# Kernel optimization log

Measured on AMD Instinct MI355X. Metric: run time of the kernel, lower is better.

The kernel has to match this reference:

```python
import jax, jax.numpy as jnp
import numpy as np
from functools import partial

EPS = 1e-5
ROPE_THETA = 10000.0
TOP_K = 2


def rmsnorm(x, w):
    # x: [..., d]
    var = jnp.mean(x * x, axis=-1, keepdims=True)
    return x * jax.lax.rsqrt(var + EPS) * w


def apply_rope(x):
    # x: [B, S, H, dh]
    B, S, H, dh = x.shape
    inv_freq = 1.0 / (ROPE_THETA ** (jnp.arange(0, dh, 2, dtype=jnp.float32) / dh))
    ang = jnp.arange(S, dtype=jnp.float32)[:, None] * inv_freq[None, :]  # [S, dh/2]
    cos = jnp.cos(ang)[None, :, None, :]
    sin = jnp.sin(ang)[None, :, None, :]
    x1 = x[..., 0::2]
    x2 = x[..., 1::2]
    r1 = x1 * cos - x2 * sin
    r2 = x1 * sin + x2 * cos
    return jnp.stack([r1, r2], axis=-1).reshape(x.shape)


def setup_inputs() -> dict:
    key = jax.random.key(0)
    B, S, D, H, E = 4, 2048, 512, 8, 8
    Hf = 4 * D  # expert FFN hidden
    ks = jax.random.split(key, 10)
    s = 0.02
    return {
        "x": jax.random.normal(ks[0], (B, S, D), dtype=jnp.float32),
        "attn_norm_w": jnp.ones((D,), dtype=jnp.float32),
        "wq": jax.random.normal(ks[1], (D, D), dtype=jnp.float32) * s,
        "wk": jax.random.normal(ks[2], (D, D), dtype=jnp.float32) * s,
        "wv": jax.random.normal(ks[3], (D, D), dtype=jnp.float32) * s,
        "wo": jax.random.normal(ks[4], (D, D), dtype=jnp.float32) * s,
        "ffn_norm_w": jnp.ones((D,), dtype=jnp.float32),
        "router_w": jax.random.normal(ks[5], (D, E), dtype=jnp.float32) * s,
        "w1": jax.random.normal(ks[6], (E, D, Hf), dtype=jnp.float32) * s,
        "w2": jax.random.normal(ks[7], (E, Hf, D), dtype=jnp.float32) * s,
    }


def mha_rope(xn, wq, wk, wv, wo, num_heads):
    B, S, D = xn.shape
    dh = D // num_heads
    q = (xn @ wq).reshape(B, S, num_heads, dh)
    k = (xn @ wk).reshape(B, S, num_heads, dh)
    v = (xn @ wv).reshape(B, S, num_heads, dh)
    q = apply_rope(q)
    k = apply_rope(k)
    scores = jnp.einsum("bqhd,bkhd->bhqk", q, k) / jnp.sqrt(jnp.float32(dh))
    causal = jnp.tril(jnp.ones((S, S), dtype=bool))
    scores = jnp.where(causal[None, None], scores, jnp.float32(-1e9))
    attn = jax.nn.softmax(scores, axis=-1)
    out = jnp.einsum("bhqk,bkhd->bqhd", attn, v).reshape(B, S, D)
    return out @ wo


def moe_ffn(hn, router_w, w1, w2):
    # hn: [B, S, D] -> tokens [T, D]; top-2 routed expert MLPs (GELU)
    B, S, D = hn.shape
    E = router_w.shape[1]
    t = hn.reshape(B * S, D)
    T = t.shape[0]
    logits = t @ router_w                      # [T, E]
    probs = jax.nn.softmax(logits, axis=-1)
    vals, idx = jax.lax.top_k(probs, TOP_K)    # [T, k]
    gates = vals / jnp.sum(vals, axis=-1, keepdims=True)
    gates_dense = jnp.zeros((T, E), dtype=t.dtype).at[
        jnp.arange(T)[:, None], idx
    ].add(gates)                               # sparse gates, zero for unrouted
    out = jnp.zeros_like(t)
    for e in range(E):  # fixed small expert loop
        ge = gates_dense[:, e:e + 1]           # [T, 1]
        h = jax.nn.gelu(t @ w1[e], approximate=False)
        out = out + ge * (h @ w2[e])
    return out.reshape(B, S, D)


def reference(x, attn_norm_w, wq, wk, wv, wo, ffn_norm_w, router_w, w1, w2):
    num_heads = 8
    h = x + mha_rope(rmsnorm(x, attn_norm_w), wq, wk, wv, wo, num_heads)
    out = h + moe_ffn(rmsnorm(h, ffn_norm_w), router_w, w1, w2)
    return out
```

## Files before the change

### kernel.cpp

```cpp
#include <hip/hip_runtime.h>

#define BATCH 4
#define SEQ 2048
#define DMODEL 512
#define NHEAD 8
#define DHEAD 64
#define NEXP 8
#define DFF 2048
#define TOK (BATCH*SEQ)

typedef __attribute__((ext_vector_type(8))) short short8;
typedef __attribute__((ext_vector_type(8))) _Float16 half8;
typedef __attribute__((ext_vector_type(4))) float f32x4;
typedef unsigned short u16;

__device__ inline f32x4 zero4(){ f32x4 z = {0.f,0.f,0.f,0.f}; return z; }
__device__ inline u16 f2bf(float f){ unsigned u; __builtin_memcpy(&u,&f,4); u = (u + 0x7fffu + ((u>>16)&1u)) >> 16; return (u16)u; }
__device__ inline unsigned pack2(_Float16 a, _Float16 b){
  unsigned short ua, ub; __builtin_memcpy(&ua,&a,2); __builtin_memcpy(&ub,&b,2);
  return (unsigned)ua | ((unsigned)ub<<16);
}

__global__ __launch_bounds__(256) void k_tc_bf(const float* __restrict__ W, u16* __restrict__ Wt, int R, int C){
  __shared__ float tile[32][33];
  long e = blockIdx.z;
  const float* Wp = W + e*(long)R*C;
  u16* Op = Wt + e*(long)R*C;
  int c0 = blockIdx.x*32, r0 = blockIdx.y*32;
  int tx = threadIdx.x & 31, ty = threadIdx.x >> 5;
  #pragma unroll
  for (int i=0;i<4;i++){ int r = ty*4+i; tile[r][tx] = Wp[(long)(r0+r)*C + c0+tx]; }
  __syncthreads();
  #pragma unroll
  for (int i=0;i<4;i++){ int cc = ty*4+i; Op[(long)(c0+cc)*R + r0+tx] = f2bf(tile[tx][cc]); }
}

__global__ __launch_bounds__(256) void k_tc_split(const float* __restrict__ W, _Float16* __restrict__ H, _Float16* __restrict__ L, int R, int C){
  __shared__ float tile[32][33];
  int c0 = blockIdx.x*32, r0 = blockIdx.y*32;
  int tx = threadIdx.x & 31, ty = threadIdx.x >> 5;
  #pragma unroll
  for (int i=0;i<4;i++){ int r = ty*4+i; tile[r][tx] = W[(long)(r0+r)*C + c0+tx]; }
  __syncthreads();
  #pragma unroll
  for (int i=0;i<4;i++){
    int cc = ty*4+i;
    float v = tile[tx][cc];
    _Float16 hi = (_Float16)v;
    long o = (long)(c0+cc)*R + r0+tx;
    H[o] = hi; L[o] = (_Float16)(v - (float)hi);
  }
}

__global__ __launch_bounds__(256) void k_vtrans(const _Float16* __restrict__ vh, const _Float16* __restrict__ vl,
                                                _Float16* __restrict__ vth, _Float16* __restrict__ vtl){
  __shared__ _Float16 t[32][33];
  int bh = blockIdx.z;
  int b = bh>>3, h = bh&7;
  int s0 = blockIdx.x*32, d0 = blockIdx.y*32;
  int tx = threadIdx.x & 31, ty = threadIdx.x >> 5;
  const _Float16* src = vh; _Float16* dst = vth;
  #pragma unroll
  for (int pass=0; pass<2; pass++){
    #pragma unroll
    for (int i=0;i<4;i++){
      int sl = ty*4+i;
      t[sl][tx] = src[((long)b*SEQ + s0+sl)*DMODEL + h*64 + d0 + tx];
    }
    __syncthreads();
    #pragma unroll
    for (int i=0;i<4;i++){
      int dl = ty*4+i;
      dst[((long)bh*64 + d0+dl)*SEQ + s0 + tx] = t[tx][dl];
    }
    __syncthreads();
    src = vl; dst = vtl;
  }
}

__global__ __launch_bounds__(256) void k_rmsnorm_split(const float* __restrict__ x, const float* __restrict__ w,
                                                       _Float16* __restrict__ oh, _Float16* __restrict__ ol){
  int row = blockIdx.x*4 + (threadIdx.x>>6);
  int lane = threadIdx.x & 63;
  const float4* xr = (const float4*)(x + (long)row*DMODEL);
  float4 a = xr[lane*2], b = xr[lane*2+1];
  float ss = a.x*a.x+a.y*a.y+a.z*a.z+a.w*a.w + b.x*b.x+b.y*b.y+b.z*b.z+b.w*b.w;
  #pragma unroll
  for (int o=32;o;o>>=1) ss += __shfl_xor(ss, o);
  float sc = rsqrtf(ss*(1.0f/DMODEL) + 1e-5f);
  const float4* wr = (const float4*)w;
  float4 wa = wr[lane*2], wb = wr[lane*2+1];
  float v[8] = {a.x*sc*wa.x, a.y*sc*wa.y, a.z*sc*wa.z, a.w*sc*wa.w,
                b.x*sc*wb.x, b.y*sc*wb.y, b.z*sc*wb.z, b.w*sc*wb.w};
  half8 hv, lv;
  #pragma unroll
  for (int j=0;j<8;j++){ _Float16 hi = (_Float16)v[j]; hv[j] = hi; lv[j] = (_Float16)(v[j]-(float)hi); }
  long off = (long)row*DMODEL + lane*8;
  *(half8*)(oh + off) = hv;
  *(half8*)(ol + off) = lv;
}

__global__ __launch_bounds__(256) void k_rmsnorm_bf(const float* __restrict__ x, const float* __restrict__ w, u16* __restrict__ o){
  int row = blockIdx.x*4 + (threadIdx.x>>6);
  int lane = threadIdx.x & 63;
  const float4* xr = (const float4*)(x + (long)row*DMODEL);
  float4 a = xr[lane*2], b = xr[lane*2+1];
  float ss = a.x*a.x+a.y*a.y+a.z*a.z+a.w*a.w + b.x*b.x+b.y*b.y+b.z*b.z+b.w*b.w;
  #pragma unroll
  for (int ofs=32;ofs;ofs>>=1) ss += __shfl_xor(ss, ofs);
  float sc = rsqrtf(ss*(1.0f/DMODEL) + 1e-5f);
  const float4* wr = (const float4*)w;
  float4 wa = wr[lane*2], wb = wr[lane*2+1];
  short8 ov;
  ov[0]=(short)f2bf(a.x*sc*wa.x); ov[1]=(short)f2bf(a.y*sc*wa.y);
  ov[2]=(short)f2bf(a.z*sc*wa.z); ov[3]=(short)f2bf(a.w*sc*wa.w);
  ov[4]=(short)f2bf(b.x*sc*wb.x); ov[5]=(short)f2bf(b.y*sc*wb.y);
  ov[6]=(short)f2bf(b.z*sc*wb.z); ov[7]=(short)f2bf(b.w*sc*wb.w);
  *(short8*)(o + (long)row*DMODEL + lane*8) = ov;
}

__global__ __launch_bounds__(256) void k_rope_tab(float2* __restrict__ tab){
  int idx = blockIdx.x*256 + threadIdx.x;
  int s = idx>>5, i = idx&31;
  float invf = powf(10000.0f, -(float)(2*i)*(1.0f/64.0f));
  float ang = (float)s * invf;
  tab[idx] = make_float2(cosf(ang), sinf(ang));
}

template<int EPI>
__global__ __launch_bounds__(256) void k_gemm_split(
    const _Float16* __restrict__ Ah, const _Float16* __restrict__ Al,
    const _Float16* __restrict__ Bh, const _Float16* __restrict__ Bl,
    _Float16* __restrict__ oh, _Float16* __restrict__ ol,
    float* __restrict__ of1, float* __restrict__ of2,
    const float* __restrict__ extra, const float2* __restrict__ tab,
    int M, int N, int K)
{
  __shared__ _Float16 lA[128*64];
  __shared__ _Float16 lB[128*64];
  const int mb = blockIdx.x*128, nb = blockIdx.y*128;
  const int tid = threadIdx.x, lane = tid&63, wid = tid>>6;
  const int wr = wid>>1, wc = wid&1;
  const int fr = lane&15, fq = lane>>4;
  const int srow = tid>>3, sch = tid&7;
  f32x4 acc[4][4];
  #pragma unroll
  for (int mi=0;mi<4;mi++)
    #pragma unroll
    for (int ni=0;ni<4;ni++) acc[mi][ni] = zero4();

  for (int kt=0; kt<K; kt+=32){
    half8 sa[4], sb[4];
    #pragma unroll
    for (int i=0;i<4;i++){
      int row = i*32 + srow;
      const _Float16* pa = (sch<4) ? Ah : Al;
      const _Float16* pb = (sch<4) ? Bh : Bl;
      sa[i] = *(const half8*)(pa + (long)(mb+row)*K + kt + (sch&3)*8);
      sb[i] = *(const half8*)(pb + (long)(nb+row)*K + kt + (sch&3)*8);
    }
    __syncthreads();
    #pragma unroll
    for (int i=0;i<4;i++){
      int row = i*32 + srow;
      int byt = row*128 + ((sch ^ (row&7))<<4);
      *(half8*)((char*)lA + byt) = sa[i];
      *(half8*)((char*)lB + byt) = sb[i];
    }
    __syncthreads();
    half8 ah[4], al[4], bh[4], bl[4];
    #pragma unroll
    for (int mi=0;mi<4;mi++){
      int row = wr*64 + mi*16 + fr; int m7 = row&7; const char* rb = (const char*)lA + row*128;
      ah[mi] = *(const half8*)(rb + (((fq  ) ^ m7)<<4));
      al[mi] = *(const half8*)(rb + (((fq+4) ^ m7)<<4));
    }
    #pragma unroll
    for (int ni=0;ni<4;ni++){
      int row = wc*64 + ni*16 + fr; int m7 = row&7; const char* rb = (const char*)lB + row*128;
      bh[ni] = *(const half8*)(rb + (((fq  ) ^ m7)<<4));
      bl[ni] = *(const half8*)(rb + (((fq+4) ^ m7)<<4));
    }
    __builtin_amdgcn_s_setprio(1);
    #pragma unroll
    for (int mi=0;mi<4;mi++)
      #pragma unroll
      for (int ni=0;ni<4;ni++){
        acc[mi][ni] = __builtin_amdgcn_mfma_f32_16x16x32_f16(ah[mi], bh[ni], acc[mi][ni], 0,0,0);
        acc[mi][ni] = __builtin_amdgcn_mfma_f32_16x16x32_f16(ah[mi], bl[ni], acc[mi][ni], 0,0,0);
        acc[mi][ni] = __builtin_amdgcn_mfma_f32_16x16x32_f16(al[mi], bh[ni], acc[mi][ni], 0,0,0);
      }
    __builtin_amdgcn_s_setprio(0);
  }
  #pragma unroll
  for (int mi=0;mi<4;mi++)
    #pragma unroll
    for (int ni=0;ni<4;ni++)
      #pragma unroll
      for (int r=0;r<4;r++){
        int row = mb + wr*64 + mi*16 + fq*4 + r;
        int col = nb + wc*64 + ni*16 + fr;
        long off = (long)row*N + col;
        float v = acc[mi][ni][r];
        if (EPI==0){
          float v2 = __shfl_xor(v, 1);
          float2 cs = tab[(row & (SEQ-1))*32 + ((col&63)>>1)];
          float o = (col&1) ? (v2*cs.y + v*cs.x) : (v*cs.x - v2*cs.y);
          _Float16 hi = (_Float16)o;
          oh[off] = hi; ol[off] = (_Float16)(o - (float)hi);
        } else if (EPI==1){
          _Float16 hi = (_Float16)v;
          oh[off] = hi; ol[off] = (_Float16)(v - (float)hi);
        } else {
          float hv = extra[off] + v;
          of1[off] = hv; of2[off] = hv;
        }
      }
}

__global__ __launch_bounds__(256) void k_flash(
    const _Float16* __restrict__ Qh, const _Float16* __restrict__ Ql,
    const _Float16* __restrict__ Kh, const _Float16* __restrict__ Kl,
    const _Float16* __restrict__ Vth, const _Float16* __restrict__ Vtl,
    _Float16* __restrict__ Oh, _Float16* __restrict__ Ol)
{
  __shared__ _Float16 lK[64*128];
  __shared__ _Float16 lV[64*128];
  __shared__ _Float16 lP[4*2304];
  const int pidx = blockIdx.x, bh = blockIdx.y;
  const int b = bh>>3, hh = bh&7;
  const int tid = threadIdx.x, lane = tid&63, wid = tid>>6;
  const int fr = lane&15, fq = lane>>4;
  const long base = ((long)b*SEQ)*DMODEL + hh*DHEAD;
  const long vtb  = (long)bh*DHEAD*SEQ;
  const int srow = tid>>4, sch = tid&15;
  const unsigned pw = wid*2304;

  for (int pass=0; pass<2; pass++){
    const int qt = pass ? (SEQ/64-1-pidx) : pidx;
    const int q0 = qt*64, qw = q0 + wid*16;
    half8 qfh[2], qfl[2];
    #pragma unroll
    for (int kk=0;kk<2;kk++){
      long o = base + (long)(qw+fr)*DMODEL + kk*32 + fq*8;
      qfh[kk] = *(const half8*)(Qh + o);
      qfl[kk] = *(const half8*)(Ql + o);
    }
    f32x4 oacc[4];
    #pragma unroll
    for (int i=0;i<4;i++) oacc[i] = zero4();
    float mrow[4], lrow[4];
    #pragma unroll
    for (int r=0;r<4;r++){ mrow[r] = -__builtin_inff(); lrow[r] = 0.f; }

    for (int kvt=0; kvt<=qt; kvt++){
      int k0 = kvt*64;
      half8 kreg[4], vreg[4];
      #pragma unroll
      for (int i=0;i<4;i++){
        int row = i*16 + srow;
        const _Float16* ks = (sch<8) ? Kh : Kl;
        kreg[i] = *(const half8*)(ks + base + (long)(k0+row)*DMODEL + (sch&7)*8);
        const _Float16* vs = (sch<8) ? Vth : Vtl;
        vreg[i] = *(const half8*)(vs + vtb + (long)row*SEQ + k0 + (sch&7)*8);
      }
      __syncthreads();
      #pragma unroll
      for (int i=0;i<4;i++){
        int row = i*16 + srow;
        int slot = ((sch ^ (row&15))<<4);
        *(half8*)((char*)lK + row*256 + slot) = kreg[i];
        *(half8*)((char*)lV + row*256 + slot) = vreg[i];
      }
      __syncthreads();
      f32x4 sc[4];
      __builtin_amdgcn_s_setprio(1);
      #pragma unroll
      for (int ns=0;ns<4;ns++){
        f32x4 a = zero4();
        #pragma unroll
        for (int kk=0;kk<2;kk++){
          int row = ns*16 + fr; int m15 = row&15; const char* rb = (const char*)lK + row*256;
          half8 kfh = *(const half8*)(rb + (((kk*4+fq)   ^ m15)<<4));
          half8 kfl = *(const half8*)(rb + (((kk*4+fq+8) ^ m15)<<4));
          a = __builtin_amdgcn_mfma_f32_16x16x32_f16(qfh[kk], kfh, a, 0,0,0);
          a = __builtin_amdgcn_mfma_f32_16x16x32_f16(qfh[kk], kfl, a, 0,0,0);
          a = __builtin_amdgcn_mfma_f32_16x16x32_f16(qfl[kk], kfh, a, 0,0,0);
        }
        sc[ns] = a;
      }
      __builtin_amdgcn_s_setprio(0);
      float pmax[4];
      #pragma unroll
      for (int r=0;r<4;r++) pmax[r] = -__builtin_inff();
      #pragma unroll
      for (int ns=0;ns<4;ns++)
        #pragma unroll
        for (int r=0;r<4;r++){
          int kvp = k0 + ns*16 + fr;
          int qp  = qw + fq*4 + r;
          float s = sc[ns][r]*0.125f;
          if (kvp > qp) s = -1e30f;
          sc[ns][r] = s;
          pmax[r] = fmaxf(pmax[r], s);
        }
      #pragma unroll
      for (int o=1;o<16;o<<=1)
        #pragma unroll
        for (int r=0;r<4;r++) pmax[r] = fmaxf(pmax[r], __shfl_xor(pmax[r], o));
      float sf[4], rsum[4] = {0,0,0,0};
      #pragma unroll
      for (int r=0;r<4;r++){
        float mn = fmaxf(mrow[r], pmax[r]);
        sf[r] = expf(mrow[r]-mn);
        mrow[r] = mn;
      }
      #pragma unroll
      for (int ns=0;ns<4;ns++)
        #pragma unroll
        for (int r=0;r<4;r++){
          float pv = expf(sc[ns][r]-mrow[r]);
          rsum[r] += pv;
          float pv2 = __shfl_xor(pv, 1);
          float e0 = (fr&1)? pv2 : pv;
          float e1 = (fr&1)? pv : pv2;
          _Float16 f0 = (_Float16)e0, f1 = (_Float16)e1;
          unsigned word;
          if (fr&1) word = pack2((_Float16)(e0-(float)f0), (_Float16)(e1-(float)f1));
          else      word = pack2(f0, f1);
          unsigned eo = pw + ((fr&1)? 1152u:0u) + (unsigned)((fq*4+r)*72 + ns*16 + (fr&~1));
          *(unsigned*)((char*)lP + eo*2) = word;
        }
      #pragma unroll
      for (int o=1;o<16;o<<=1)
        #pragma unroll
        for (int r=0;r<4;r++) rsum[r] += __shfl_xor(rsum[r], o);
      #pragma unroll
      for (int r=0;r<4;r++) lrow[r] = lrow[r]*sf[r] + rsum[r];
      #pragma unroll
      for (int dt=0;dt<4;dt++)
        #pragma unroll
        for (int r=0;r<4;r++) oacc[dt][r] *= sf[r];
      __builtin_amdgcn_s_setprio(1);
      #pragma unroll
      for (int kk=0;kk<2;kk++){
        const char* pb = (const char*)lP + (pw + (unsigned)(fr*72 + kk*32))*2;
        half8 pfh = *(const half8*)(pb + fq*16);
        half8 pfl = *(const half8*)(pb + 2304 + fq*16);
        #pragma unroll
        for (int dt=0;dt<4;dt++){
          int row = dt*16 + fr; int m15 = row&15; const char* vb = (const char*)lV + row*256;
          half8 vfh = *(const half8*)(vb + (((kk*4+fq)   ^ m15)<<4));
          half8 vfl = *(const half8*)(vb + (((kk*4+fq+8) ^ m15)<<4));
          oacc[dt] = __builtin_amdgcn_mfma_f32_16x16x32_f16(pfh, vfh, oacc[dt], 0,0,0);
          oacc[dt] = __builtin_amdgcn_mfma_f32_16x16x32_f16(pfh, vfl, oacc[dt], 0,0,0);
          oacc[dt] = __builtin_amdgcn_mfma_f32_16x16x32_f16(pfl, vfh, oacc[dt], 0,0,0);
        }
      }
      __builtin_amdgcn_s_setprio(0);
    }
    #pragma unroll
    for (int dt=0;dt<4;dt++)
      #pragma unroll
      for (int r=0;r<4;r++){
        int qp = qw + fq*4 + r;
        float ov = oacc[dt][r] / lrow[r];
        long o = base + (long)qp*DMODEL + dt*16 + fr;
        _Float16 hi = (_Float16)ov;
        Oh[o] = hi; Ol[o] = (_Float16)(ov - (float)hi);
      }
    __syncthreads();
  }
}

__global__ __launch_bounds__(256) void k_router(const float* __restrict__ h, const float* __restrict__ w,
                                                const float* __restrict__ rw, float* __restrict__ gates,
                                                unsigned* __restrict__ choice){
  int tok = blockIdx.x*4 + (threadIdx.x>>6);
  int lane = threadIdx.x & 63;
  const float4* xr = (const float4*)(h + (long)tok*DMODEL);
  float4 a = xr[lane*2], b = xr[lane*2+1];
  float ss = a.x*a.x+a.y*a.y+a.z*a.z+a.w*a.w + b.x*b.x+b.y*b.y+b.z*b.z+b.w*b.w;
  #pragma unroll
  for (int o=32;o;o>>=1) ss += __shfl_xor(ss, o);
  float sc = rsqrtf(ss*(1.0f/DMODEL) + 1e-5f);
  const float4* wr = (const float4*)w;
  float4 wa = wr[lane*2], wb = wr[lane*2+1];
  float xv[8] = {a.x*sc*wa.x, a.y*sc*wa.y, a.z*sc*wa.z, a.w*sc*wa.w,
                 b.x*sc*wb.x, b.y*sc*wb.y, b.z*sc*wb.z, b.w*sc*wb.w};
  float lg[8] = {0,0,0,0,0,0,0,0};
  #pragma unroll
  for (int j=0;j<8;j++){
    const float* rp = rw + (long)(lane*8+j)*NEXP;
    #pragma unroll
    for (int e=0;e<8;e++) lg[e] += xv[j]*rp[e];
  }
  #pragma unroll
  for (int o=1;o<64;o<<=1)
    #pragma unroll
    for (int e=0;e<8;e++) lg[e] += __shfl_xor(lg[e], o);
  float mx = lg[0];
  #pragma unroll
  for (int e=1;e<8;e++) mx = fmaxf(mx, lg[e]);
  float pe[8], sm = 0.f;
  #pragma unroll
  for (int e=0;e<8;e++){ pe[e] = expf(lg[e]-mx); sm += pe[e]; }
  #pragma unroll
  for (int e=0;e<8;e++) pe[e] /= sm;
  int e1 = 0; float p1 = pe[0];
  #pragma unroll
  for (int e=1;e<8;e++) if (pe[e] > p1){ p1 = pe[e]; e1 = e; }
  int e2 = -1; float p2 = -1.f;
  #pragma unroll
  for (int e=0;e<8;e++) if (e != e1 && pe[e] > p2){ p2 = pe[e]; e2 = e; }
  float gs = p1 + p2;
  if (lane == 0){
    #pragma unroll
    for (int e=0;e<8;e++)
      gates[(long)tok*NEXP + e] = (e==e1) ? (p1/gs) : ((e==e2) ? (p2/gs) : 0.f);
    choice[tok] = (unsigned)e1 | ((unsigned)e2<<8);
  }
}

__global__ __launch_bounds__(256) void k_build(const unsigned* __restrict__ choice,
                                               int* __restrict__ cnt, int* __restrict__ perm){
  __shared__ int lcnt[NEXP];
  __shared__ int lbase[NEXP];
  const int tid = threadIdx.x;
  const int tok = blockIdx.x*256 + tid;
  if (tid < NEXP) lcnt[tid] = 0;
  __syncthreads();
  unsigned ch = choice[tok];
  int e1 = ch & 0xff, e2 = (ch>>8) & 0xff;
  int p1 = atomicAdd(&lcnt[e1], 1);
  int p2 = atomicAdd(&lcnt[e2], 1);
  __syncthreads();
  if (tid < NEXP) lbase[tid] = atomicAdd(&cnt[tid], lcnt[tid]);
  __syncthreads();
  perm[e1*TOK + lbase[e1] + p1] = tok;
  perm[e2*TOK + lbase[e2] + p2] = tok;
}

__global__ void k_prefix(const int* __restrict__ cnt, int* __restrict__ baseP){
  if (threadIdx.x==0 && blockIdx.x==0){
    int run = 0;
    for (int e=0;e<NEXP;e++){ baseP[e] = run; run += (cnt[e]+127) & ~127; }
  }
}

__global__ __launch_bounds__(256) void k_moe1(
    const u16* __restrict__ A, const u16* __restrict__ W1, u16* __restrict__ mid,
    const int* __restrict__ perm, const int* __restrict__ cnt, const int* __restrict__ baseP)
{
  const int e = blockIdx.z;
  const int ce = cnt[e];
  const int mb = blockIdx.x*128;
  if (mb >= ce) return;
  const int bp = baseP[e];
  const u16* Bt = W1 + (size_t)e*DFF*DMODEL;
  const int nb = blockIdx.y*128;
  __shared__ u16 lA[128*64];
  __shared__ u16 lB[128*64];
  const int tid = threadIdx.x, lane = tid&63, wid = tid>>6;
  const int wr = wid>>1, wc = wid&1;
  const int fr = lane&15, fq = lane>>4;
  const int srow = tid>>3, sch = tid&7;
  int toks[4];
  #pragma unroll
  for (int i=0;i<4;i++){
    int r = mb + i*32 + srow;
    toks[i] = perm[e*TOK + (r < ce ? r : ce-1)];
  }
  f32x4 acc[4][4];
  #pragma unroll
  for (int mi=0;mi<4;mi++)
    #pragma unroll
    for (int ni=0;ni<4;ni++) acc[mi][ni] = zero4();

  for (int kt=0; kt<DMODEL; kt+=64){
    short8 sa[4], sb[4];
    #pragma unroll
    for (int i=0;i<4;i++){
      sa[i] = *(const short8*)(A  + (long)toks[i]*DMODEL + kt + sch*8);
      sb[i] = *(const short8*)(Bt + (long)(nb + i*32 + srow)*DMODEL + kt + sch*8);
    }
    __syncthreads();
    #pragma unroll
    for (int i=0;i<4;i++){
      int row = i*32 + srow;
      int byt = row*128 + ((sch ^ (row&7))<<4);
      *(short8*)((char*)lA + byt) = sa[i];
      *(short8*)((char*)lB + byt) = sb[i];
    }
    __syncthreads();
    __builtin_amdgcn_s_setprio(1);
    #pragma unroll
    for (int kk=0;kk<2;kk++){
      short8 af[4], bff[4];
      #pragma unroll
      for (int mi=0;mi<4;mi++){
        int row = wr*64 + mi*16 + fr;
        af[mi] = *(const short8*)((char*)lA + row*128 + (((kk*4+fq) ^ (row&7))<<4));
      }
      #pragma unroll
      for (int ni=0;ni<4;ni++){
        int row = wc*64 + ni*16 + fr;
        bff[ni] = *(const short8*)((char*)lB + row*128 + (((kk*4+fq) ^ (row&7))<<4));
      }
      #pragma unroll
      for (int mi=0;mi<4;mi++)
        #pragma unroll
        for (int ni=0;ni<4;ni++)
          acc[mi][ni] = __builtin_amdgcn_mfma_f32_16x16x32_bf16(af[mi], bff[ni], acc[mi][ni], 0,0,0);
    }
    __builtin_amdgcn_s_setprio(0);
  }
  #pragma unroll
  for (int mi=0;mi<4;mi++)
    #pragma unroll
    for (int ni=0;ni<4;ni++)
      #pragma unroll
      for (int r=0;r<4;r++){
        int row_loc = mb + wr*64 + mi*16 + fq*4 + r;
        int col = nb + wc*64 + ni*16 + fr;
        float v = acc[mi][ni][r];
        mid[(size_t)(bp + row_loc)*DFF + col] = f2bf(0.5f*v*(1.f + erff(v*0.7071067811865475f)));
      }
}

__global__ __launch_bounds__(256) void k_moe2(
    const u16* __restrict__ mid, const u16* __restrict__ W2, float* __restrict__ out,
    const int* __restrict__ perm, const int* __restrict__ cnt, const int* __restrict__ baseP,
    const float* __restrict__ gates)
{
  const int e = blockIdx.z;
  const int ce = cnt[e];
  const int mb = blockIdx.x*128;
  if (mb >= ce) return;
  const int bp = baseP[e];
  const u16* Bt = W2 + (size_t)e*DMODEL*DFF;
  const int nb = blockIdx.y*128;
  __shared__ u16 lA[128*64];
  __shared__ u16 lB[128*64];
  const int tid = threadIdx.x, lane = tid&63, wid = tid>>6;
  const int wr = wid>>1, wc = wid&1;
  const int fr = lane&15, fq = lane>>4;
  const int srow = tid>>3, sch = tid&7;
  f32x4 acc[4][4];
  #pragma unroll
  for (int mi=0;mi<4;mi++)
    #pragma unroll
    for (int ni=0;ni<4;ni++) acc[mi][ni] = zero4();

  for (int kt=0; kt<DFF; kt+=64){
    short8 sa[4], sb[4];
    #pragma unroll
    for (int i=0;i<4;i++){
      sa[i] = *(const short8*)(mid + (size_t)(bp + mb + i*32 + srow)*DFF + kt + sch*8);
      sb[i] = *(const short8*)(Bt  + (long)(nb + i*32 + srow)*DFF + kt + sch*8);
    }
    __syncthreads();
    #pragma unroll
    for (int i=0;i<4;i++){
      int row = i*32 + srow;
      int byt = row*128 + ((sch ^ (row&7))<<4);
      *(short8*)((char*)lA + byt) = sa[i];
      *(short8*)((char*)lB + byt) = sb[i];
    }
    __syncthreads();
    __builtin_amdgcn_s_setprio(1);
    #pragma unroll
    for (int kk=0;kk<2;kk++){
      short8 af[4], bff[4];
      #pragma unroll
      for (int mi=0;mi<4;mi++){
        int row = wr*64 + mi*16 + fr;
        af[mi] = *(const short8*)((char*)lA + row*128 + (((kk*4+fq) ^ (row&7))<<4));
      }
      #pragma unroll
      for (int ni=0;ni<4;ni++){
        int row = wc*64 + ni*16 + fr;
        bff[ni] = *(const short8*)((char*)lB + row*128 + (((kk*4+fq) ^ (row&7))<<4));
      }
      #pragma unroll
      for (int mi=0;mi<4;mi++)
        #pragma unroll
        for (int ni=0;ni<4;ni++)
          acc[mi][ni] = __builtin_amdgcn_mfma_f32_16x16x32_bf16(af[mi], bff[ni], acc[mi][ni], 0,0,0);
    }
    __builtin_amdgcn_s_setprio(0);
  }
  #pragma unroll
  for (int mi=0;mi<4;mi++)
    #pragma unroll
    for (int ni=0;ni<4;ni++)
      #pragma unroll
      for (int r=0;r<4;r++){
        int row_loc = mb + wr*64 + mi*16 + fq*4 + r;
        if (row_loc < ce){
          int tok = perm[e*TOK + row_loc];
          int col = nb + wc*64 + ni*16 + fr;
          float g = gates[(long)tok*NEXP + e];
          atomicAdd(out + (long)tok*DMODEL + col, g*acc[mi][ni][r]);
        }
      }
}

extern "C" void kernel_launch(void* const* d_in, const int* in_sizes, int n_in,
                              void* d_out, int out_size, void* d_ws, size_t ws_size,
                              hipStream_t stream)
{
  const float* x   = (const float*)d_in[0];
  const float* anw = (const float*)d_in[1];
  const float* wq  = (const float*)d_in[2];
  const float* wk  = (const float*)d_in[3];
  const float* wv  = (const float*)d_in[4];
  const float* wo  = (const float*)d_in[5];
  const float* fnw = (const float*)d_in[6];
  const float* rw  = (const float*)d_in[7];
  const float* w1  = (const float*)d_in[8];
  const float* w2  = (const float*)d_in[9];
  float* out = (float*)d_out;

  char* p = (char*)d_ws;
  auto alloc = [&](size_t n){ char* r = p; p += (n + 255) & ~(size_t)255; return r; };
  _Float16* xnh = (_Float16*)alloc((size_t)TOK*DMODEL*2);
  _Float16* xnl = (_Float16*)alloc((size_t)TOK*DMODEL*2);
  _Float16* qh  = (_Float16*)alloc((size_t)TOK*DMODEL*2);
  _Float16* ql  = (_Float16*)alloc((size_t)TOK*DMODEL*2);
  _Float16* kh  = (_Float16*)alloc((size_t)TOK*DMODEL*2);
  _Float16* kl  = (_Float16*)alloc((size_t)TOK*DMODEL*2);
  _Float16* vh  = (_Float16*)alloc((size_t)TOK*DMODEL*2);
  _Float16* vl  = (_Float16*)alloc((size_t)TOK*DMODEL*2);
  _Float16* vth = (_Float16*)alloc((size_t)TOK*DMODEL*2);
  _Float16* vtl = (_Float16*)alloc((size_t)TOK*DMODEL*2);
  u16* hmid = (u16*)xnh;
  _Float16* wqTh = (_Float16*)alloc((size_t)DMODEL*DMODEL*2);
  _Float16* wqTl = (_Float16*)alloc((size_t)DMODEL*DMODEL*2);
  _Float16* wkTh = (_Float16*)alloc((size_t)DMODEL*DMODEL*2);
  _Float16* wkTl = (_Float16*)alloc((size_t)DMODEL*DMODEL*2);
  _Float16* wvTh = (_Float16*)alloc((size_t)DMODEL*DMODEL*2);
  _Float16* wvTl = (_Float16*)alloc((size_t)DMODEL*DMODEL*2);
  _Float16* woTh = (_Float16*)alloc((size_t)DMODEL*DMODEL*2);
  _Float16* woTl = (_Float16*)alloc((size_t)DMODEL*DMODEL*2);
  u16* w1T = (u16*)alloc((size_t)NEXP*DFF*DMODEL*2);
  u16* w2T = (u16*)alloc((size_t)NEXP*DMODEL*DFF*2);
  _Float16* aoh = (_Float16*)alloc((size_t)TOK*DMODEL*2);
  _Float16* aol = (_Float16*)alloc((size_t)TOK*DMODEL*2);
  float* hb  = (float*)alloc((size_t)TOK*DMODEL*4);
  u16* hnb   = (u16*)alloc((size_t)TOK*DMODEL*2);
  float2* tab = (float2*)alloc((size_t)SEQ*32*sizeof(float2));
  float* gates = (float*)alloc((size_t)TOK*NEXP*4);
  int* perm  = (int*)alloc((size_t)NEXP*TOK*4);
  unsigned* choice = (unsigned*)alloc((size_t)TOK*4);
  int* cnt   = (int*)alloc(64*4);
  int* baseP = (int*)alloc(64*4);

  dim3 blk(256);
  hipMemsetAsync(cnt, 0, NEXP*sizeof(int), stream);
  k_tc_split<<<dim3(16,16,1), blk, 0, stream>>>(wq, wqTh, wqTl, DMODEL, DMODEL);
  k_tc_split<<<dim3(16,16,1), blk, 0, stream>>>(wk, wkTh, wkTl, DMODEL, DMODEL);
  k_tc_split<<<dim3(16,16,1), blk, 0, stream>>>(wv, wvTh, wvTl, DMODEL, DMODEL);
  k_tc_split<<<dim3(16,16,1), blk, 0, stream>>>(wo, woTh, woTl, DMODEL, DMODEL);
  k_tc_bf<<<dim3(DFF/32, DMODEL/32, NEXP), blk, 0, stream>>>(w1, w1T, DMODEL, DFF);
  k_tc_bf<<<dim3(DMODEL/32, DFF/32, NEXP), blk, 0, stream>>>(w2, w2T, DFF, DMODEL);
  k_rope_tab<<<dim3(SEQ*32/256), blk, 0, stream>>>(tab);
  k_rmsnorm_split<<<dim3(TOK/4), blk, 0, stream>>>(x, anw, xnh, xnl);
  k_gemm_split<0><<<dim3(TOK/128, DMODEL/128), blk, 0, stream>>>(xnh, xnl, wqTh, wqTl, qh, ql, nullptr, nullptr, nullptr, tab, TOK, DMODEL, DMODEL);
  k_gemm_split<0><<<dim3(TOK/128, DMODEL/128), blk, 0, stream>>>(xnh, xnl, wkTh, wkTl, kh, kl, nullptr, nullptr, nullptr, tab, TOK, DMODEL, DMODEL);
  k_gemm_split<1><<<dim3(TOK/128, DMODEL/128), blk, 0, stream>>>(xnh, xnl, wvTh, wvTl, vh, vl, nullptr, nullptr, nullptr, nullptr, TOK, DMODEL, DMODEL);
  k_vtrans<<<dim3(SEQ/32, 2, BATCH*NHEAD), blk, 0, stream>>>(vh, vl, vth, vtl);
  k_flash<<<dim3(SEQ/128, BATCH*NHEAD), blk, 0, stream>>>(qh, ql, kh, kl, vth, vtl, aoh, aol);
  k_gemm_split<2><<<dim3(TOK/128, DMODEL/128), blk, 0, stream>>>(aoh, aol, woTh, woTl, nullptr, nullptr, hb, out, x, nullptr, TOK, DMODEL, DMODEL);
  k_router<<<dim3(TOK/4), blk, 0, stream>>>(hb, fnw, rw, gates, choice);
  k_build<<<dim3(TOK/256), blk, 0, stream>>>(choice, cnt, perm);
  k_prefix<<<dim3(1), dim3(64), 0, stream>>>(cnt, baseP);
  k_rmsnorm_bf<<<dim3(TOK/4), blk, 0, stream>>>(hb, fnw, hnb);
  k_moe1<<<dim3(TOK/128, DFF/128, NEXP), blk, 0, stream>>>(hnb, w1T, hmid, perm, cnt, baseP);
  k_moe2<<<dim3(TOK/128, DMODEL/128, NEXP), blk, 0, stream>>>(hmid, w2T, out, perm, cnt, baseP, gates);
}
```

Baseline: 743.2 us.

## Use direct global-to-LDS loads, double-buffer GEMM, restructure flash attention scheduling

The split-precision GEMM and both MoE GEMMs now stage tiles with global_load_lds (direct global-to-LDS copies) instead of going through registers, and the split GEMM double-buffers its LDS tiles so the next tile loads while the current one computes. The flash attention kernel drops its two-pass pairing and launches one q-tile per block, with the largest tiles scheduled first. It also applies causal masking only on the diagonal tile, switches to exp2 with the log2e factor folded into the scale, and rescales the running max only when it grows by more than a threshold. These aim to cut register staging and sync stalls and to reduce softmax work, at the cost of more LDS use in the GEMM and a looser running-max update.

```diff
diff --git a/kernel.cpp b/kernel.cpp
--- a/kernel.cpp
+++ b/kernel.cpp
@@ -13,6 +13,12 @@
 typedef __attribute__((ext_vector_type(8))) _Float16 half8;
 typedef __attribute__((ext_vector_type(4))) float f32x4;
 typedef unsigned short u16;
+
+typedef const __attribute__((address_space(1))) void gvoid;
+typedef __attribute__((address_space(3))) void lvoid;
+__device__ __forceinline__ void gload16(const void* g, void* l){
+  __builtin_amdgcn_global_load_lds((gvoid*)g, (lvoid*)l, 16, 0, 0);
+}
 
 __device__ inline f32x4 zero4(){ f32x4 z = {0.f,0.f,0.f,0.f}; return z; }
 __device__ inline u16 f2bf(float f){ unsigned u; __builtin_memcpy(&u,&f,4); u = (u + 0x7fffu + ((u>>16)&1u)) >> 16; return (u16)u; }
@@ -136,61 +142,73 @@
     const float* __restrict__ extra, const float2* __restrict__ tab,
     int M, int N, int K)
 {
-  __shared__ _Float16 lA[128*64];
-  __shared__ _Float16 lB[128*64];
+  __shared__ _Float16 lAb[2*128*64];
+  __shared__ _Float16 lBb[2*128*64];
   const int mb = blockIdx.x*128, nb = blockIdx.y*128;
-  const int tid = threadIdx.x, lane = tid&63, wid = tid>>6;
-  const int wr = wid>>1, wc = wid&1;
+  const int tid = threadIdx.x, lane = tid&63, wv = tid>>6;
+  const int wr = wv>>1, wc = wv&1;
   const int fr = lane&15, fq = lane>>4;
-  const int srow = tid>>3, sch = tid&7;
+  const int cs = (lane&7) ^ (lane>>3);
+  const _Float16* pA[4]; const _Float16* pB[4];
+  #pragma unroll
+  for (int i=0;i<4;i++){
+    int rr = i*32 + wv*8 + (lane>>3);
+    const _Float16* a = (cs<4)? Ah : Al;
+    const _Float16* b = (cs<4)? Bh : Bl;
+    pA[i] = a + (long)(mb+rr)*K + (cs&3)*8;
+    pB[i] = b + (long)(nb+rr)*K + (cs&3)*8;
+  }
   f32x4 acc[4][4];
   #pragma unroll
   for (int mi=0;mi<4;mi++)
     #pragma unroll
     for (int ni=0;ni<4;ni++) acc[mi][ni] = zero4();
 
-  for (int kt=0; kt<K; kt+=32){
-    half8 sa[4], sb[4];
-    #pragma unroll
-    for (int i=0;i<4;i++){
-      int row = i*32 + srow;
-      const _Float16* pa = (sch<4) ? Ah : Al;
-      const _Float16* pb = (sch<4) ? Bh : Bl;
-      sa[i] = *(const half8*)(pa + (long)(mb+row)*K + kt + (sch&3)*8);
-      sb[i] = *(const half8*)(pb + (long)(nb+row)*K + kt + (sch&3)*8);
-    }
-    __syncthreads();
-    #pragma unroll
-    for (int i=0;i<4;i++){
-      int row = i*32 + srow;
-      int byt = row*128 + ((sch ^ (row&7))<<4);
-      *(half8*)((char*)lA + byt) = sa[i];
-      *(half8*)((char*)lB + byt) = sb[i];
-    }
-    __syncthreads();
-    half8 ah[4], al[4], bh[4], bl[4];
+  #pragma unroll
+  for (int i=0;i<4;i++){
+    gload16(pA[i], (char*)lAb + (i*32+wv*8)*128);
+    gload16(pB[i], (char*)lBb + (i*32+wv*8)*128);
+  }
+  __syncthreads();
+  const int NT = K>>5;
+  int cur = 0;
+  for (int t=0; t<NT; ++t){
+    if (t+1 < NT){
+      int k2 = (t+1)<<5;
+      #pragma unroll
+      for (int i=0;i<4;i++){
+        int db = ((cur^1)<<14) + (i*32+wv*8)*128;
+        gload16(pA[i]+k2, (char*)lAb + db);
+        gload16(pB[i]+k2, (char*)lBb + db);
+      }
+    }
+    const char* cA = (const char*)lAb + (cur<<14);
+    const char* cB = (const char*)lBb + (cur<<14);
+    half8 ax[4], ay[4], bx[4], by[4];
     #pragma unroll
     for (int mi=0;mi<4;mi++){
-      int row = wr*64 + mi*16 + fr; int m7 = row&7; const char* rb = (const char*)lA + row*128;
-      ah[mi] = *(const half8*)(rb + (((fq  ) ^ m7)<<4));
-      al[mi] = *(const half8*)(rb + (((fq+4) ^ m7)<<4));
+      int row = wr*64 + mi*16 + fr; int m7 = row&7; const char* rb = cA + row*128;
+      ax[mi] = *(const half8*)(rb + (((fq  ) ^ m7)<<4));
+      ay[mi] = *(const half8*)(rb + (((fq+4) ^ m7)<<4));
     }
     #pragma unroll
     for (int ni=0;ni<4;ni++){
-      int row = wc*64 + ni*16 + fr; int m7 = row&7; const char* rb = (const char*)lB + row*128;
-      bh[ni] = *(const half8*)(rb + (((fq  ) ^ m7)<<4));
-      bl[ni] = *(const half8*)(rb + (((fq+4) ^ m7)<<4));
+      int row = wc*64 + ni*16 + fr; int m7 = row&7; const char* rb = cB + row*128;
+      bx[ni] = *(const half8*)(rb + (((fq  ) ^ m7)<<4));
+      by[ni] = *(const half8*)(rb + (((fq+4) ^ m7)<<4));
     }
     __builtin_amdgcn_s_setprio(1);
     #pragma unroll
     for (int mi=0;mi<4;mi++)
       #pragma unroll
       for (int ni=0;ni<4;ni++){
-        acc[mi][ni] = __builtin_amdgcn_mfma_f32_16x16x32_f16(ah[mi], bh[ni], acc[mi][ni], 0,0,0);
-        acc[mi][ni] = __builtin_amdgcn_mfma_f32_16x16x32_f16(ah[mi], bl[ni], acc[mi][ni], 0,0,0);
-        acc[mi][ni] = __builtin_amdgcn_mfma_f32_16x16x32_f16(al[mi], bh[ni], acc[mi][ni], 0,0,0);
+        acc[mi][ni] = __builtin_amdgcn_mfma_f32_16x16x32_f16(ax[mi], bx[ni], acc[mi][ni], 0,0,0);
+        acc[mi][ni] = __builtin_amdgcn_mfma_f32_16x16x32_f16(ax[mi], by[ni], acc[mi][ni], 0,0,0);
+        acc[mi][ni] = __builtin_amdgcn_mfma_f32_16x16x32_f16(ay[mi], bx[ni], acc[mi][ni], 0,0,0);
       }
     __builtin_amdgcn_s_setprio(0);
+    __syncthreads();
+    cur ^= 1;
   }
   #pragma unroll
   for (int mi=0;mi<4;mi++)
@@ -204,8 +222,8 @@
         float v = acc[mi][ni][r];
         if (EPI==0){
           float v2 = __shfl_xor(v, 1);
-          float2 cs = tab[(row & (SEQ-1))*32 + ((col&63)>>1)];
-          float o = (col&1) ? (v2*cs.y + v*cs.x) : (v*cs.x - v2*cs.y);
+          float2 csn = tab[(row & (SEQ-1))*32 + ((col&63)>>1)];
+          float o = (col&1) ? (v2*csn.y + v*csn.x) : (v*csn.x - v2*csn.y);
           _Float16 hi = (_Float16)o;
           oh[off] = hi; ol[off] = (_Float16)(o - (float)hi);
         } else if (EPI==1){
@@ -227,7 +245,8 @@
   __shared__ _Float16 lK[64*128];
   __shared__ _Float16 lV[64*128];
   __shared__ _Float16 lP[4*2304];
-  const int pidx = blockIdx.x, bh = blockIdx.y;
+  const int qt = (SEQ/64 - 1) - blockIdx.x;
+  const int bh = blockIdx.y;
   const int b = bh>>3, hh = bh&7;
   const int tid = threadIdx.x, lane = tid&63, wid = tid>>6;
   const int fr = lane&15, fq = lane>>4;
@@ -235,142 +254,157 @@
   const long vtb  = (long)bh*DHEAD*SEQ;
   const int srow = tid>>4, sch = tid&15;
   const unsigned pw = wid*2304;
-
-  for (int pass=0; pass<2; pass++){
-    const int qt = pass ? (SEQ/64-1-pidx) : pidx;
-    const int q0 = qt*64, qw = q0 + wid*16;
-    half8 qfh[2], qfl[2];
-    #pragma unroll
-    for (int kk=0;kk<2;kk++){
-      long o = base + (long)(qw+fr)*DMODEL + kk*32 + fq*8;
-      qfh[kk] = *(const half8*)(Qh + o);
-      qfl[kk] = *(const half8*)(Ql + o);
-    }
-    f32x4 oacc[4];
-    #pragma unroll
-    for (int i=0;i<4;i++) oacc[i] = zero4();
-    float mrow[4], lrow[4];
-    #pragma unroll
-    for (int r=0;r<4;r++){ mrow[r] = -__builtin_inff(); lrow[r] = 0.f; }
-
-    for (int kvt=0; kvt<=qt; kvt++){
-      int k0 = kvt*64;
-      half8 kreg[4], vreg[4];
-      #pragma unroll
-      for (int i=0;i<4;i++){
-        int row = i*16 + srow;
-        const _Float16* ks = (sch<8) ? Kh : Kl;
-        kreg[i] = *(const half8*)(ks + base + (long)(k0+row)*DMODEL + (sch&7)*8);
-        const _Float16* vs = (sch<8) ? Vth : Vtl;
-        vreg[i] = *(const half8*)(vs + vtb + (long)row*SEQ + k0 + (sch&7)*8);
-      }
-      __syncthreads();
-      #pragma unroll
-      for (int i=0;i<4;i++){
-        int row = i*16 + srow;
-        int slot = ((sch ^ (row&15))<<4);
-        *(half8*)((char*)lK + row*256 + slot) = kreg[i];
-        *(half8*)((char*)lV + row*256 + slot) = vreg[i];
-      }
-      __syncthreads();
-      f32x4 sc[4];
-      __builtin_amdgcn_s_setprio(1);
-      #pragma unroll
-      for (int ns=0;ns<4;ns++){
-        f32x4 a = zero4();
-        #pragma unroll
-        for (int kk=0;kk<2;kk++){
-          int row = ns*16 + fr; int m15 = row&15; const char* rb = (const char*)lK + row*256;
-          half8 kfh = *(const half8*)(rb + (((kk*4+fq)   ^ m15)<<4));
-          half8 kfl = *(const half8*)(rb + (((kk*4+fq+8) ^ m15)<<4));
-          a = __builtin_amdgcn_mfma_f32_16x16x32_f16(qfh[kk], kfh, a, 0,0,0);
-          a = __builtin_amdgcn_mfma_f32_16x16x32_f16(qfh[kk], kfl, a, 0,0,0);
-          a = __builtin_amdgcn_mfma_f32_16x16x32_f16(qfl[kk], kfh, a, 0,0,0);
-        }
-        sc[ns] = a;
-      }
-      __builtin_amdgcn_s_setprio(0);
-      float pmax[4];
-      #pragma unroll
-      for (int r=0;r<4;r++) pmax[r] = -__builtin_inff();
+  const float SCL = 0.18033688011112042f;
+
+  const int q0 = qt*64, qw = q0 + wid*16;
+  half8 qfh[2], qfl[2];
+  #pragma unroll
+  for (int kk=0;kk<2;kk++){
+    long o = base + (long)(qw+fr)*DMODEL + kk*32 + fq*8;
+    qfh[kk] = *(const half8*)(Qh + o);
+    qfl[kk] = *(const half8*)(Ql + o);
+  }
+  f32x4 oacc[4];
+  #pragma unroll
+  for (int i=0;i<4;i++) oacc[i] = zero4();
+  float mrow[4], lrow[4];
+  #pragma unroll
+  for (int r=0;r<4;r++){ mrow[r] = -__builtin_inff(); lrow[r] = 0.f; }
+
+  for (int kvt=0; kvt<=qt; kvt++){
+    int k0 = kvt*64;
+    half8 kreg[4], vreg[4];
+    #pragma unroll
+    for (int i=0;i<4;i++){
+      int row = i*16 + srow;
+      const _Float16* ks = (sch<8) ? Kh : Kl;
+      kreg[i] = *(const half8*)(ks + base + (long)(k0+row)*DMODEL + (sch&7)*8);
+      const _Float16* vs = (sch<8) ? Vth : Vtl;
+      vreg[i] = *(const half8*)(vs + vtb + (long)row*SEQ + k0 + (sch&7)*8);
+    }
+    __syncthreads();
+    #pragma unroll
+    for (int i=0;i<4;i++){
+      int row = i*16 + srow;
+      int slot = ((sch ^ (row&15))<<4);
+      *(half8*)((char*)lK + row*256 + slot) = kreg[i];
+      *(half8*)((char*)lV + row*256 + slot) = vreg[i];
+    }
+    __syncthreads();
+    f32x4 sc[4];
+    __builtin_amdgcn_s_setprio(1);
+    #pragma unroll
+    for (int ns=0;ns<4;ns++){
+      f32x4 a = zero4();
+      #pragma unroll
+      for (int kk=0;kk<2;kk++){
+        int row = ns*16 + fr; int m15 = row&15; const char* rb = (const char*)lK + row*256;
+        half8 kfh = *(const half8*)(rb + (((kk*4+fq)   ^ m15)<<4));
+        half8 kfl = *(const half8*)(rb + (((kk*4+fq+8) ^ m15)<<4));
+        a = __builtin_amdgcn_mfma_f32_16x16x32_f16(qfh[kk], kfh, a, 0,0,0);
+        a = __builtin_amdgcn_mfma_f32_16x16x32_f16(qfh[kk], kfl, a, 0,0,0);
+        a = __builtin_amdgcn_mfma_f32_16x16x32_f16(qfl[kk], kfh, a, 0,0,0);
+      }
+      sc[ns] = a;
+    }
+    __builtin_amdgcn_s_setprio(0);
+    float pmax[4];
+    #pragma unroll
+    for (int r=0;r<4;r++) pmax[r] = -__builtin_inff();
+    if (kvt == qt){
       #pragma unroll
       for (int ns=0;ns<4;ns++)
         #pragma unroll
         for (int r=0;r<4;r++){
           int kvp = k0 + ns*16 + fr;
           int qp  = qw + fq*4 + r;
-          float s = sc[ns][r]*0.125f;
+          float s = sc[ns][r]*SCL;
           if (kvp > qp) s = -1e30f;
           sc[ns][r] = s;
           pmax[r] = fmaxf(pmax[r], s);
         }
-      #pragma unroll
-      for (int o=1;o<16;o<<=1)
-        #pragma unroll
-        for (int r=0;r<4;r++) pmax[r] = fmaxf(pmax[r], __shfl_xor(pmax[r], o));
-      float sf[4], rsum[4] = {0,0,0,0};
-      #pragma unroll
-      for (int r=0;r<4;r++){
-        float mn = fmaxf(mrow[r], pmax[r]);
-        sf[r] = expf(mrow[r]-mn);
-        mrow[r] = mn;
-      }
+    } else {
       #pragma unroll
       for (int ns=0;ns<4;ns++)
         #pragma unroll
         for (int r=0;r<4;r++){
-          float pv = expf(sc[ns][r]-mrow[r]);
-          rsum[r] += pv;
-          float pv2 = __shfl_xor(pv, 1);
-          float e0 = (fr&1)? pv2 : pv;
-          float e1 = (fr&1)? pv : pv2;
-          _Float16 f0 = (_Float16)e0, f1 = (_Float16)e1;
-          unsigned word;
-          if (fr&1) word = pack2((_Float16)(e0-(float)f0), (_Float16)(e1-(float)f1));
-          else      word = pack2(f0, f1);
-          unsigned eo = pw + ((fr&1)? 1152u:0u) + (unsigned)((fq*4+r)*72 + ns*16 + (fr&~1));
-          *(unsigned*)((char*)lP + eo*2) = word;
+          float s = sc[ns][r]*SCL;
+          sc[ns][r] = s;
+          pmax[r] = fmaxf(pmax[r], s);
         }
-      #pragma unroll
-      for (int o=1;o<16;o<<=1)
-        #pragma unroll
-        for (int r=0;r<4;r++) rsum[r] += __shfl_xor(rsum[r], o);
-      #pragma unroll
-      for (int r=0;r<4;r++) lrow[r] = lrow[r]*sf[r] + rsum[r];
+    }
+    #pragma unroll
+    for (int o=1;o<16;o<<=1)
+      #pragma unroll
+      for (int r=0;r<4;r++) pmax[r] = fmaxf(pmax[r], __shfl_xor(pmax[r], o));
+    bool need = false;
+    #pragma unroll
+    for (int r=0;r<4;r++) need = need || (pmax[r] > mrow[r] + 10.f);
+    if (__any(need)){
+      float sf[4];
+      #pragma unroll
+      for (int r=0;r<4;r++){
+        float mn = fmaxf(mrow[r], pmax[r]);
+        sf[r] = exp2f(mrow[r]-mn);
+        mrow[r] = mn;
+        lrow[r] *= sf[r];
+      }
       #pragma unroll
       for (int dt=0;dt<4;dt++)
         #pragma unroll
         for (int r=0;r<4;r++) oacc[dt][r] *= sf[r];
-      __builtin_amdgcn_s_setprio(1);
-      #pragma unroll
-      for (int kk=0;kk<2;kk++){
-        const char* pb = (const char*)lP + (pw + (unsigned)(fr*72 + kk*32))*2;
-        half8 pfh = *(const half8*)(pb + fq*16);
-        half8 pfl = *(const half8*)(pb + 2304 + fq*16);
-        #pragma unroll
-        for (int dt=0;dt<4;dt++){
-          int row = dt*16 + fr; int m15 = row&15; const char* vb = (const char*)lV + row*256;
-          half8 vfh = *(const half8*)(vb + (((kk*4+fq)   ^ m15)<<4));
-          half8 vfl = *(const half8*)(vb + (((kk*4+fq+8) ^ m15)<<4));
-          oacc[dt] = __builtin_amdgcn_mfma_f32_16x16x32_f16(pfh, vfh, oacc[dt], 0,0,0);
-          oacc[dt] = __builtin_amdgcn_mfma_f32_16x16x32_f16(pfh, vfl, oacc[dt], 0,0,0);
-          oacc[dt] = __builtin_amdgcn_mfma_f32_16x16x32_f16(pfl, vfh, oacc[dt], 0,0,0);
-        }
-      }
-      __builtin_amdgcn_s_setprio(0);
-    }
-    #pragma unroll
-    for (int dt=0;dt<4;dt++)
+    }
+    float rsum[4] = {0,0,0,0};
+    #pragma unroll
+    for (int ns=0;ns<4;ns++)
       #pragma unroll
       for (int r=0;r<4;r++){
-        int qp = qw + fq*4 + r;
-        float ov = oacc[dt][r] / lrow[r];
-        long o = base + (long)qp*DMODEL + dt*16 + fr;
-        _Float16 hi = (_Float16)ov;
-        Oh[o] = hi; Ol[o] = (_Float16)(ov - (float)hi);
-      }
-    __syncthreads();
-  }
+        float pv = exp2f(sc[ns][r]-mrow[r]);
+        rsum[r] += pv;
+        float pv2 = __shfl_xor(pv, 1);
+        float e0 = (fr&1)? pv2 : pv;
+        float e1 = (fr&1)? pv : pv2;
+        _Float16 f0 = (_Float16)e0, f1 = (_Float16)e1;
+        unsigned word;
+        if (fr&1) word = pack2((_Float16)(e0-(float)f0), (_Float16)(e1-(float)f1));
+        else      word = pack2(f0, f1);
+        unsigned eo = pw + ((fr&1)? 1152u:0u) + (unsigned)((fq*4+r)*72 + ns*16 + (fr&~1));
+        *(unsigned*)((char*)lP + eo*2) = word;
+      }
+    #pragma unroll
+    for (int o=1;o<16;o<<=1)
+      #pragma unroll
+      for (int r=0;r<4;r++) rsum[r] += __shfl_xor(rsum[r], o);
+    #pragma unroll
+    for (int r=0;r<4;r++) lrow[r] += rsum[r];
+    __builtin_amdgcn_s_setprio(1);
+    #pragma unroll
+    for (int kk=0;kk<2;kk++){
+      const char* pb = (const char*)lP + (pw + (unsigned)(fr*72 + kk*32))*2;
+      half8 pfh = *(const half8*)(pb + fq*16);
+      half8 pfl = *(const half8*)(pb + 2304 + fq*16);
+      #pragma unroll
+      for (int dt=0;dt<4;dt++){
+        int row = dt*16 + fr; int m15 = row&15; const char* vb = (const char*)lV + row*256;
+        half8 vfh = *(const half8*)(vb + (((kk*4+fq)   ^ m15)<<4));
+        half8 vfl = *(const half8*)(vb + (((kk*4+fq+8) ^ m15)<<4));
+        oacc[dt] = __builtin_amdgcn_mfma_f32_16x16x32_f16(pfh, vfh, oacc[dt], 0,0,0);
+        oacc[dt] = __builtin_amdgcn_mfma_f32_16x16x32_f16(pfh, vfl, oacc[dt], 0,0,0);
+        oacc[dt] = __builtin_amdgcn_mfma_f32_16x16x32_f16(pfl, vfh, oacc[dt], 0,0,0);
+      }
+    }
+    __builtin_amdgcn_s_setprio(0);
+  }
+  #pragma unroll
+  for (int dt=0;dt<4;dt++)
+    #pragma unroll
+    for (int r=0;r<4;r++){
+      int qp = qw + fq*4 + r;
+      float ov = oacc[dt][r] / lrow[r];
+      long o = base + (long)qp*DMODEL + dt*16 + fr;
+      _Float16 hi = (_Float16)ov;
+      Oh[o] = hi; Ol[o] = (_Float16)(ov - (float)hi);
+    }
 }
 
 __global__ __launch_bounds__(256) void k_router(const float* __restrict__ h, const float* __restrict__ w,
@@ -461,15 +495,17 @@
   const int nb = blockIdx.y*128;
   __shared__ u16 lA[128*64];
   __shared__ u16 lB[128*64];
-  const int tid = threadIdx.x, lane = tid&63, wid = tid>>6;
-  const int wr = wid>>1, wc = wid&1;
+  const int tid = threadIdx.x, lane = tid&63, wv = tid>>6;
+  const int wr = wv>>1, wc = wv&1;
   const int fr = lane&15, fq = lane>>4;
-  const int srow = tid>>3, sch = tid&7;
-  int toks[4];
+  const int cs = (lane&7) ^ (lane>>3);
+  const u16* pA[4]; const u16* pB[4];
   #pragma unroll
   for (int i=0;i<4;i++){
-    int r = mb + i*32 + srow;
-    toks[i] = perm[e*TOK + (r < ce ? r : ce-1)];
+    int rr = mb + i*32 + wv*8 + (lane>>3);
+    int tok = perm[e*TOK + (rr < ce ? rr : ce-1)];
+    pA[i] = A  + (long)tok*DMODEL + cs*8;
+    pB[i] = Bt + (long)(nb + i*32 + wv*8 + (lane>>3))*DMODEL + cs*8;
   }
   f32x4 acc[4][4];
   #pragma unroll
@@ -478,19 +514,10 @@
     for (int ni=0;ni<4;ni++) acc[mi][ni] = zero4();
 
   for (int kt=0; kt<DMODEL; kt+=64){
-    short8 sa[4], sb[4];
     #pragma unroll
     for (int i=0;i<4;i++){
-      sa[i] = *(const short8*)(A  + (long)toks[i]*DMODEL + kt + sch*8);
-      sb[i] = *(const short8*)(Bt + (long)(nb + i*32 + srow)*DMODEL + kt + sch*8);
-    }
-    __syncthreads();
-    #pragma unroll
-    for (int i=0;i<4;i++){
-      int row = i*32 + srow;
-      int byt = row*128 + ((sch ^ (row&7))<<4);
-      *(short8*)((char*)lA + byt) = sa[i];
-      *(short8*)((char*)lB + byt) = sb[i];
+      gload16(pA[i]+kt, (char*)lA + (i*32+wv*8)*128);
+      gload16(pB[i]+kt, (char*)lB + (i*32+wv*8)*128);
     }
     __syncthreads();
     __builtin_amdgcn_s_setprio(1);
@@ -514,6 +541,7 @@
           acc[mi][ni] = __builtin_amdgcn_mfma_f32_16x16x32_bf16(af[mi], bff[ni], acc[mi][ni], 0,0,0);
     }
     __builtin_amdgcn_s_setprio(0);
+    __syncthreads();
   }
   #pragma unroll
   for (int mi=0;mi<4;mi++)
@@ -542,10 +570,17 @@
   const int nb = blockIdx.y*128;
   __shared__ u16 lA[128*64];
   __shared__ u16 lB[128*64];
-  const int tid = threadIdx.x, lane = tid&63, wid = tid>>6;
-  const int wr = wid>>1, wc = wid&1;
+  const int tid = threadIdx.x, lane = tid&63, wv = tid>>6;
+  const int wr = wv>>1, wc = wv&1;
   const int fr = lane&15, fq = lane>>4;
-  const int srow = tid>>3, sch = tid&7;
+  const int cs = (lane&7) ^ (lane>>3);
+  const u16* pA[4]; const u16* pB[4];
+  #pragma unroll
+  for (int i=0;i<4;i++){
+    int rr = i*32 + wv*8 + (lane>>3);
+    pA[i] = mid + (size_t)(bp + mb + rr)*DFF + cs*8;
+    pB[i] = Bt  + (long)(nb + rr)*DFF + cs*8;
+  }
   f32x4 acc[4][4];
   #pragma unroll
   for (int mi=0;mi<4;mi++)
@@ -553,19 +588,10 @@
     for (int ni=0;ni<4;ni++) acc[mi][ni] = zero4();
 
   for (int kt=0; kt<DFF; kt+=64){
-    short8 sa[4], sb[4];
     #pragma unroll
     for (int i=0;i<4;i++){
-      sa[i] = *(const short8*)(mid + (size_t)(bp + mb + i*32 + srow)*DFF + kt + sch*8);
-      sb[i] = *(const short8*)(Bt  + (long)(nb + i*32 + srow)*DFF + kt + sch*8);
-    }
-    __syncthreads();
-    #pragma unroll
-    for (int i=0;i<4;i++){
-      int row = i*32 + srow;
-      int byt = row*128 + ((sch ^ (row&7))<<4);
-      *(short8*)((char*)lA + byt) = sa[i];
-      *(short8*)((char*)lB + byt) = sb[i];
+      gload16(pA[i]+kt, (char*)lA + (i*32+wv*8)*128);
+      gload16(pB[i]+kt, (char*)lB + (i*32+wv*8)*128);
     }
     __syncthreads();
     __builtin_amdgcn_s_setprio(1);
@@ -589,6 +615,7 @@
           acc[mi][ni] = __builtin_amdgcn_mfma_f32_16x16x32_bf16(af[mi], bff[ni], acc[mi][ni], 0,0,0);
     }
     __builtin_amdgcn_s_setprio(0);
+    __syncthreads();
   }
   #pragma unroll
   for (int mi=0;mi<4;mi++)
@@ -670,7 +697,7 @@
   k_gemm_split<0><<<dim3(TOK/128, DMODEL/128), blk, 0, stream>>>(xnh, xnl, wkTh, wkTl, kh, kl, nullptr, nullptr, nullptr, tab, TOK, DMODEL, DMODEL);
   k_gemm_split<1><<<dim3(TOK/128, DMODEL/128), blk, 0, stream>>>(xnh, xnl, wvTh, wvTl, vh, vl, nullptr, nullptr, nullptr, nullptr, TOK, DMODEL, DMODEL);
   k_vtrans<<<dim3(SEQ/32, 2, BATCH*NHEAD), blk, 0, stream>>>(vh, vl, vth, vtl);
-  k_flash<<<dim3(SEQ/128, BATCH*NHEAD), blk, 0, stream>>>(qh, ql, kh, kl, vth, vtl, aoh, aol);
+  k_flash<<<dim3(SEQ/64, BATCH*NHEAD), blk, 0, stream>>>(qh, ql, kh, kl, vth, vtl, aoh, aol);
   k_gemm_split<2><<<dim3(TOK/128, DMODEL/128), blk, 0, stream>>>(aoh, aol, woTh, woTl, nullptr, nullptr, hb, out, x, nullptr, TOK, DMODEL, DMODEL);
   k_router<<<dim3(TOK/4), blk, 0, stream>>>(hb, fnw, rw, gates, choice);
   k_build<<<dim3(TOK/256), blk, 0, stream>>>(choice, cnt, perm);
```

Result: slower. 760.8 us (+2.4%).
